# Kernel optimization log

Measured on AMD Instinct MI355X. Metric: run time of the kernel, lower is better.

The kernel has to match this reference:

```python
import jax, jax.numpy as jnp
import numpy as np
import math

B, T, C = 4, 2048, 1024
H, D = 16, 64            # num_heads, head_dim
ORIG_LEN = 4096
MIN_FREQ, MAX_FREQ = 0.5, 40.0


def setup_inputs() -> dict:
    key = jax.random.key(0)
    ks = jax.random.split(key, 6)
    x = jax.random.normal(ks[0], (B, T, C), dtype=jnp.float32)
    keep_idx = jnp.sort(jax.random.randint(ks[1], (B, T, 1), 0, ORIG_LEN), axis=1)
    W_qkv = jax.random.normal(ks[2], (C, 3 * C), dtype=jnp.float32) * (1.0 / math.sqrt(C))
    b_qkv = jnp.zeros((3 * C,), dtype=jnp.float32)
    W_proj = jax.random.normal(ks[3], (C, C), dtype=jnp.float32) * (1.0 / math.sqrt(C))
    b_proj = jnp.zeros((C,), dtype=jnp.float32)
    return {"x": x, "keep_idx": keep_idx, "original_seq_len": ORIG_LEN,
            "W_qkv": W_qkv, "b_qkv": b_qkv, "W_proj": W_proj, "b_proj": b_proj}


def _rope_angles(positions, orig_len):
    # positions: [b, t] float token positions in the ORIGINAL sequence.
    # golden_gate 1-D RoPE: normalized positions times geometric frequency band.
    half = D // 2
    freqs = MIN_FREQ * (MAX_FREQ / MIN_FREQ) ** (jnp.arange(half, dtype=jnp.float32) / (half - 1))
    pos_norm = positions / jnp.float32(orig_len)          # [b, t]
    return 2.0 * jnp.pi * pos_norm[:, :, None] * freqs    # [b, t, half]


def _apply_rope(x, cos, sin):
    # x: [b, h, t, d]; cos/sin: [b, 1, t, d/2]; rotate (first half, second half) pairs
    half = D // 2
    x1, x2 = x[..., :half], x[..., half:]
    return jnp.concatenate([x1 * cos - x2 * sin, x1 * sin + x2 * cos], axis=-1)


def reference(x, keep_idx, original_seq_len, W_qkv, b_qkv, W_proj, b_proj):
    b, t, c = x.shape
    # fused QKV projection + head split: (b,t,3c) -> (b,t,3,h,d) -> (b,h,t,3,d)
    qkv = (x @ W_qkv + b_qkv).reshape(b, t, 3, H, D).transpose(0, 3, 1, 2, 4)
    q, k, v = qkv[:, :, :, 0], qkv[:, :, :, 1], qkv[:, :, :, 2]  # each [b,h,t,d]

    positions = keep_idx[..., 0].astype(jnp.float32)             # [b, t]
    ang = _rope_angles(positions, original_seq_len)              # [b, t, d/2]
    cos = jnp.cos(ang)[:, None]                                  # [b,1,t,d/2]
    sin = jnp.sin(ang)[:, None]
    q = _apply_rope(q, cos, sin)
    k = _apply_rope(k, cos, sin)

    # dense non-causal scaled dot-product attention
    scale = 1.0 / math.sqrt(D)
    scores = jnp.einsum('bhqd,bhkd->bhqk', q, k) * scale
    attn = jax.nn.softmax(scores, axis=-1)
    out = jnp.einsum('bhqk,bhkd->bhqd', attn, v)                 # [b,h,t,d]

    out = out.transpose(0, 2, 1, 3).reshape(b, t, H * D)         # [b,t,c]
    return out @ W_proj + b_proj
```

## Files before the change

### kernel.cpp

```cpp
#include <hip/hip_runtime.h>
#include <hip/hip_bf16.h>
#include <math.h>

#define B_ 4
#define T_ 2048
#define C_ 1024
#define H_ 16
#define D_ 64

typedef __attribute__((ext_vector_type(8))) short bf16x8_t;
typedef __attribute__((ext_vector_type(4))) float f32x4_t;
typedef __attribute__((ext_vector_type(2))) unsigned int uiv2_t;

#define SHIFT2 32.0f

#define GLOAD_LDS16(gp, lp)                                                          \
    __builtin_amdgcn_global_load_lds(                                                \
        (const __attribute__((address_space(1))) void*)(gp),                         \
        (__attribute__((address_space(3))) void*)(lp), 16, 0, 0)

#define WAVE_ORDER() __builtin_amdgcn_wave_barrier()

__device__ inline unsigned int pack2bf(float a, float b) {
    __hip_bfloat162 h = __float22bfloat162_rn(make_float2(a, b));
    return *reinterpret_cast<unsigned int*>(&h);
}

__global__ __launch_bounds__(256)
void prep_kernel(const float* __restrict__ x, __hip_bfloat16* __restrict__ xbf,
                 const int* __restrict__ keep, const int* __restrict__ orig,
                 float* __restrict__ tab,
                 const float* __restrict__ Wqkv, __hip_bfloat16* __restrict__ WqkvT,
                 const float* __restrict__ Wproj, __hip_bfloat16* __restrict__ WprojT) {
    __shared__ float s[32][33];
    const int bid = blockIdx.x;
    const int tid = threadIdx.x;

    if (bid < 8192) {
        int i = bid * 256 + tid;
        float4 v = *(const float4*)(x + (size_t)i * 4);
        uint2 u;
        u.x = pack2bf(v.x, v.y);
        u.y = pack2bf(v.z, v.w);
        *(uint2*)(xbf + (size_t)i * 4) = u;
    } else if (bid < 9216) {
        int i = (bid - 8192) * 256 + tid;
        int tok = i >> 5, d = i & 31;
        float freq = 0.5f * exp2f((float)d * (6.321928094887362f / 31.0f));
        float ang  = 6.283185307179586f * ((float)keep[tok] / (float)(*orig)) * freq;
        tab[(size_t)tok * 64 + d]      = cosf(ang);
        tab[(size_t)tok * 64 + 32 + d] = sinf(ang);
    } else {
        const float* in;
        __hip_bfloat16* outp;
        int N, n0, k0, r;
        if (bid < 12288) {
            r = bid - 9216;
            in = Wqkv; outp = WqkvT; N = 3 * C_;
            n0 = (r % 96) * 32; k0 = (r / 96) * 32;
        } else {
            r = bid - 12288;
            in = Wproj; outp = WprojT; N = C_;
            n0 = (r % 32) * 32; k0 = (r / 32) * 32;
        }
        const int K = C_;
        const int tx = tid & 31;
        const int ty = tid >> 5;
#pragma unroll
        for (int yy = 0; yy < 32; yy += 8)
            s[ty + yy][tx] = in[(size_t)(k0 + ty + yy) * N + n0 + tx];
        __syncthreads();
#pragma unroll
        for (int yy = 0; yy < 32; yy += 8)
            outp[(size_t)(n0 + ty + yy) * K + k0 + tx] = __float2bfloat16(s[tx][ty + yy]);
    }
}

#define ATILE (256 * 32)
#define BTILE (128 * 32)

template <int MODE>
__global__ __launch_bounds__(512)
void gemm_kernel(const __hip_bfloat16* __restrict__ A,
                 const __hip_bfloat16* __restrict__ BT,
                 const float* __restrict__ bias,
                 float* __restrict__ out,
                 __hip_bfloat16* __restrict__ qbuf,
                 __hip_bfloat16* __restrict__ kbuf,
                 __hip_bfloat16* __restrict__ vtbuf,
                 const float* __restrict__ ropetab,
                 int M, int N, int K) {
    __shared__ __align__(16) __hip_bfloat16 GS[2 * ATILE + 2 * BTILE];

    const int tid  = threadIdx.x;
    const int lane = tid & 63;
    const int wave = tid >> 6;
    const int wm   = wave >> 1;
    const int wn   = wave & 1;
    const int l15  = lane & 15;
    const int quad = lane >> 4;

    const int nT  = N >> 7;
    const int grp = blockIdx.x / (8 * nT);
    const int rem = blockIdx.x - grp * 8 * nT;
    const int m0  = (grp * 8 + (rem & 7)) * 256;
    const int n0  = (rem >> 3) * 128;

    f32x4_t acc[4][4];
#pragma unroll
    for (int i = 0; i < 4; i++)
#pragma unroll
        for (int j = 0; j < 4; j++) acc[i][j] = (f32x4_t)0.0f;

    const int lrow = lane >> 2;
    const int scol = ((lane & 3) ^ ((lane >> 4) & 3)) * 8;
    const __hip_bfloat16* gA  = A  + (size_t)(m0 + wave * 32 + lrow) * K + scol;
    const __hip_bfloat16* gA2 = gA + (size_t)16 * K;
    const __hip_bfloat16* gB  = BT + (size_t)(n0 + wave * 16 + lrow) * K + scol;
    const int ldsA = wave * 32 * 32;
    const int ldsB = wave * 16 * 32;

    const int NK = K >> 5;
    GLOAD_LDS16(gA,  GS + ldsA);
    GLOAD_LDS16(gA2, GS + ldsA + 16 * 32);
    GLOAD_LDS16(gB,  GS + 2 * ATILE + ldsB);

    for (int t = 0; t < NK; ++t) {
        const int Ab = (t & 1) * ATILE;
        const int Bb = 2 * ATILE + (t & 1) * BTILE;
        if (t + 1 < NK) {
            const int An = (~t & 1) * ATILE;
            const int Bn = 2 * ATILE + (~t & 1) * BTILE;
            const int kk = (t + 1) << 5;
            GLOAD_LDS16(gA  + kk, GS + An + ldsA);
            GLOAD_LDS16(gA2 + kk, GS + An + ldsA + 16 * 32);
            GLOAD_LDS16(gB  + kk, GS + Bn + ldsB);
            asm volatile("s_waitcnt vmcnt(3)" ::: "memory");
        } else {
            asm volatile("s_waitcnt vmcnt(0)" ::: "memory");
        }
        __builtin_amdgcn_s_barrier();
        __builtin_amdgcn_sched_barrier(0);

        bf16x8_t af[4], bfv[4];
#pragma unroll
        for (int i = 0; i < 4; i++)
            af[i] = *(const bf16x8_t*)(GS + Ab + (wm * 64 + i * 16 + l15) * 32 +
                                       ((quad ^ (l15 >> 2)) * 8));
#pragma unroll
        for (int j = 0; j < 4; j++)
            bfv[j] = *(const bf16x8_t*)(GS + Bb + (wn * 64 + j * 16 + l15) * 32 +
                                        ((quad ^ (l15 >> 2)) * 8));
#pragma unroll
        for (int i = 0; i < 4; i++)
#pragma unroll
            for (int j = 0; j < 4; j++)
                acc[i][j] = __builtin_amdgcn_mfma_f32_16x16x32_bf16(af[i], bfv[j], acc[i][j], 0, 0, 0);

        __builtin_amdgcn_sched_barrier(0);
        asm volatile("s_waitcnt lgkmcnt(0)" ::: "memory");
        __builtin_amdgcn_s_barrier();
    }

    float bv[4];
#pragma unroll
    for (int j = 0; j < 4; j++)
        bv[j] = bias[n0 + wn * 64 + j * 16 + l15];

    if (MODE == 0) {
#pragma unroll
        for (int i = 0; i < 4; i++)
#pragma unroll
            for (int r = 0; r < 4; r++) {
                int row = m0 + wm * 64 + i * 16 + quad * 4 + r;
#pragma unroll
                for (int j = 0; j < 4; j++) {
                    int col = n0 + wn * 64 + j * 16 + l15;
                    out[(size_t)row * N + col] = acc[i][j][r] + bv[j];
                }
            }
    } else {
        const int cb   = n0 + wn * 64;
        const int part = cb >> 10;
        if (part == 2) {
            const int hb = (n0 & 1023) >> 6;
            const int bb = m0 >> 11;
            const int t0 = m0 & 2047;
            __hip_bfloat16* L = GS;
#pragma unroll
            for (int p = 0; p < 2; ++p) {
                if ((wm >> 1) == p) {
#pragma unroll
                    for (int j = 0; j < 4; j++) {
                        int d = wn * 64 + j * 16 + l15;
#pragma unroll
                        for (int i = 0; i < 4; i++) {
                            int rtb = (wm & 1) * 64 + i * 16 + quad * 4;
                            uint2 pk;
                            pk.x = pack2bf(acc[i][j][0] + bv[j], acc[i][j][1] + bv[j]);
                            pk.y = pack2bf(acc[i][j][2] + bv[j], acc[i][j][3] + bv[j]);
                            *(uint2*)(L + d * 136 + rtb) = pk;
                        }
                    }
                }
                __syncthreads();
                {
                    int row = tid >> 2;
                    int hb2 = hb + (row >> 6);
                    int dd  = row & 63;
                    const __hip_bfloat16* src = L + row * 136;
                    __hip_bfloat16* dstv = vtbuf +
                        ((size_t)((bb * H_ + hb2) * D_ + dd)) * T_ + t0 + p * 128;
#pragma unroll
                    for (int s2 = 0; s2 < 4; s2++) {
                        int ch = (tid & 3) + s2 * 4;
                        *(bf16x8_t*)(dstv + ch * 8) = *(const bf16x8_t*)(src + ch * 8);
                    }
                }
                if (p == 0) __syncthreads();
            }
        } else {
            const int h = (cb & 1023) >> 6;
            __hip_bfloat16* dst = (part == 0) ? qbuf : kbuf;
            const float sc = (part == 0) ? 0.18033688011112042f : 1.0f;
#pragma unroll
            for (int i = 0; i < 4; i++) {
#pragma unroll
                for (int r = 0; r < 4; r++) {
                    int row = m0 + wm * 64 + i * 16 + quad * 4 + r;
                    int b = row >> 11;
                    int t = row & 2047;
                    const float* trow = ropetab + (size_t)row * 64;
                    size_t base = ((size_t)(b * H_ + h) * T_ + t) * D_;
#pragma unroll
                    for (int j = 0; j < 2; j++) {
                        int d = j * 16 + l15;
                        float cs = trow[d];
                        float sn = trow[32 + d];
                        float x1 = acc[i][j][r]     + bv[j];
                        float x2 = acc[i][j + 2][r] + bv[j + 2];
                        dst[base + d]      = __float2bfloat16(sc * (x1 * cs - x2 * sn));
                        dst[base + d + 32] = __float2bfloat16(sc * (x1 * sn + x2 * cs));
                    }
                }
            }
        }
    }
}

#define KVTILE (64 * 64)

__global__ __launch_bounds__(256, 4)
void attn_kernel(const __hip_bfloat16* __restrict__ q,
                 const __hip_bfloat16* __restrict__ k,
                 const __hip_bfloat16* __restrict__ vt,
                 __hip_bfloat16* __restrict__ attn_out) {
    __shared__ __align__(16) __hip_bfloat16 SMEM[4 * KVTILE];

    const int tid  = threadIdx.x;
    const int lane = tid & 63;
    const int wave = tid >> 6;
    const int l15  = lane & 15;
    const int quad = lane >> 4;
    const int x7   = l15 & 7;

    const int bh = blockIdx.x & 63;
    const int qt = blockIdx.x >> 6;
    const int b  = bh >> 4;
    const int h  = bh & 15;

    const size_t qkbase = (size_t)bh * T_ * D_;
    const size_t vbase  = (size_t)bh * D_ * T_;
    const int    qrow0  = qt * 128 + wave * 32;

    const int drow   = lane >> 3;
    const int gchunk = (lane & 7) ^ drow;

    const __hip_bfloat16* kg = k + qkbase;
    const __hip_bfloat16* vg = vt + vbase;

    const int c0 = ((quad)     ^ x7) * 8;
    const int c1 = ((4 + quad) ^ x7) * 8;

    bf16x8_t qa[2][2];
#pragma unroll
    for (int qf = 0; qf < 2; qf++)
#pragma unroll
        for (int kk = 0; kk < 2; kk++)
            qa[qf][kk] = *(const bf16x8_t*)(q + qkbase +
                          (size_t)(qrow0 + qf * 16 + l15) * D_ + kk * 32 + quad * 8);

    bf16x8_t ones;
#pragma unroll
    for (int i = 0; i < 8; i++) ones[i] = (short)0x3F80;

    const f32x4_t mbias = (f32x4_t)(-SHIFT2);

    f32x4_t o[2][4];
#pragma unroll
    for (int qf = 0; qf < 2; qf++)
#pragma unroll
        for (int jd = 0; jd < 4; jd++) o[qf][jd] = (f32x4_t)0.0f;
    f32x4_t osum[2];
    osum[0] = (f32x4_t)0.0f;
    osum[1] = (f32x4_t)0.0f;

#pragma unroll
    for (int i = 0; i < 2; i++) {
        int r = wave * 16 + i * 8;
        GLOAD_LDS16(kg + (size_t)(r + drow) * D_ + gchunk * 8, SMEM + r * 64);
        GLOAD_LDS16(vg + (size_t)(r + drow) * T_ + gchunk * 8, SMEM + 2 * KVTILE + r * 64);
    }

    for (int kt = 0; kt < T_ / 64; kt++) {
        const int curoff = (kt & 1) * KVTILE;
        const int nxtoff = curoff ^ KVTILE;
        if (kt + 1 < T_ / 64) {
#pragma unroll
            for (int i = 0; i < 2; i++) {
                int r = wave * 16 + i * 8;
                GLOAD_LDS16(kg + (size_t)((kt + 1) * 64 + r + drow) * D_ + gchunk * 8,
                            SMEM + nxtoff + r * 64);
                GLOAD_LDS16(vg + (size_t)(r + drow) * T_ + (kt + 1) * 64 + gchunk * 8,
                            SMEM + 2 * KVTILE + nxtoff + r * 64);
            }
            asm volatile("s_waitcnt vmcnt(4)" ::: "memory");
        } else {
            asm volatile("s_waitcnt vmcnt(0)" ::: "memory");
        }
        __builtin_amdgcn_s_barrier();
        __builtin_amdgcn_sched_barrier(0);

        const __hip_bfloat16* KLc = SMEM + curoff;
        const __hip_bfloat16* VLc = SMEM + 2 * KVTILE + curoff;

        bf16x8_t kf[4][2];
#pragma unroll
        for (int jt = 0; jt < 4; jt++) {
            kf[jt][0] = *(const bf16x8_t*)(KLc + (jt * 16 + l15) * 64 + c0);
            kf[jt][1] = *(const bf16x8_t*)(KLc + (jt * 16 + l15) * 64 + c1);
        }

        f32x4_t sT[2][4];
        __builtin_amdgcn_s_setprio(1);
#pragma unroll
        for (int jt = 0; jt < 4; jt++)
#pragma unroll
            for (int qf = 0; qf < 2; qf++) {
                sT[qf][jt] = __builtin_amdgcn_mfma_f32_16x16x32_bf16(
                    kf[jt][0], qa[qf][0], mbias, 0, 0, 0);
                sT[qf][jt] = __builtin_amdgcn_mfma_f32_16x16x32_bf16(
                    kf[jt][1], qa[qf][1], sT[qf][jt], 0, 0, 0);
            }
        __builtin_amdgcn_s_setprio(0);

        bf16x8_t pb[2][2];
#pragma unroll
        for (int qf = 0; qf < 2; qf++) {
            unsigned int w0[4], w1[4];
#pragma unroll
            for (int jt = 0; jt < 4; jt++) {
                float p0 = __builtin_amdgcn_exp2f(sT[qf][jt][0]);
                float p1 = __builtin_amdgcn_exp2f(sT[qf][jt][1]);
                float p2 = __builtin_amdgcn_exp2f(sT[qf][jt][2]);
                float p3 = __builtin_amdgcn_exp2f(sT[qf][jt][3]);
                w0[jt] = pack2bf(p0, p1);
                w1[jt] = pack2bf(p2, p3);
            }
#pragma unroll
            for (int kk = 0; kk < 2; kk++) {
                uiv2_t s0 = __builtin_amdgcn_permlane32_swap(w0[2 * kk], w0[2 * kk + 1], false, false);
                uiv2_t r0 = __builtin_amdgcn_permlane16_swap(s0[0], s0[1], false, false);
                uiv2_t s1 = __builtin_amdgcn_permlane32_swap(w1[2 * kk], w1[2 * kk + 1], false, false);
                uiv2_t r1 = __builtin_amdgcn_permlane16_swap(s1[0], s1[1], false, false);
                union { unsigned int u[4]; bf16x8_t v; } pu;
                pu.u[0] = r0[0];
                pu.u[1] = r1[0];
                pu.u[2] = r0[1];
                pu.u[3] = r1[1];
                pb[qf][kk] = pu.v;
            }
        }

        __builtin_amdgcn_s_setprio(1);
#pragma unroll
        for (int qf = 0; qf < 2; qf++) {
            osum[qf] = __builtin_amdgcn_mfma_f32_16x16x32_bf16(ones, pb[qf][0], osum[qf], 0, 0, 0);
            osum[qf] = __builtin_amdgcn_mfma_f32_16x16x32_bf16(ones, pb[qf][1], osum[qf], 0, 0, 0);
        }

#pragma unroll
        for (int jd = 0; jd < 4; jd++) {
            bf16x8_t vf0 = *(const bf16x8_t*)(VLc + (jd * 16 + l15) * 64 + c0);
            bf16x8_t vf1 = *(const bf16x8_t*)(VLc + (jd * 16 + l15) * 64 + c1);
#pragma unroll
            for (int qf = 0; qf < 2; qf++) {
                o[qf][jd] = __builtin_amdgcn_mfma_f32_16x16x32_bf16(vf0, pb[qf][0], o[qf][jd], 0, 0, 0);
                o[qf][jd] = __builtin_amdgcn_mfma_f32_16x16x32_bf16(vf1, pb[qf][1], o[qf][jd], 0, 0, 0);
            }
        }
        __builtin_amdgcn_s_setprio(0);

        __builtin_amdgcn_sched_barrier(0);
        asm volatile("s_waitcnt lgkmcnt(0)" ::: "memory");
        __builtin_amdgcn_s_barrier();
    }

    float inv[2];
    inv[0] = 1.0f / osum[0][0];
    inv[1] = 1.0f / osum[1][0];

    __hip_bfloat16* Pep = SMEM + wave * (32 * 72);

    WAVE_ORDER();
#pragma unroll
    for (int qf = 0; qf < 2; qf++) {
#pragma unroll
        for (int jd = 0; jd < 4; jd++) {
            uint2 pk;
            pk.x = pack2bf(o[qf][jd][0] * inv[qf], o[qf][jd][1] * inv[qf]);
            pk.y = pack2bf(o[qf][jd][2] * inv[qf], o[qf][jd][3] * inv[qf]);
            *(uint2*)(Pep + (qf * 16 + l15) * 72 + jd * 16 + quad * 4) = pk;
        }
    }
    WAVE_ORDER();

#pragma unroll
    for (int rnd = 0; rnd < 4; rnd++) {
        int row = rnd * 8 + (lane >> 3);
        int col = (lane & 7) * 8;
        bf16x8_t vrow = *(const bf16x8_t*)(Pep + row * 72 + col);
        int token = qt * 128 + wave * 32 + row;
        *(bf16x8_t*)(attn_out + ((size_t)(b * T_ + token)) * C_ + h * 64 + col) = vrow;
    }
}

extern "C" void kernel_launch(void* const* d_in, const int* in_sizes, int n_in,
                              void* d_out, int out_size, void* d_ws, size_t ws_size,
                              hipStream_t stream) {
    const float* x        = (const float*)d_in[0];
    const int*   keep_idx = (const int*)d_in[1];
    const int*   orig_len = (const int*)d_in[2];
    const float* Wqkv     = (const float*)d_in[3];
    const float* bqkv     = (const float*)d_in[4];
    const float* Wproj    = (const float*)d_in[5];
    const float* bproj    = (const float*)d_in[6];
    float*       out      = (float*)d_out;

    const size_t NTOK = (size_t)B_ * T_;
    const size_t QKV1 = NTOK * C_;

    __hip_bfloat16* qbuf    = (__hip_bfloat16*)d_ws;
    __hip_bfloat16* kbuf    = qbuf    + QKV1;
    __hip_bfloat16* vtbuf   = kbuf    + QKV1;
    __hip_bfloat16* attnbuf = vtbuf   + QKV1;
    __hip_bfloat16* WqkvT   = attnbuf + QKV1;
    __hip_bfloat16* WprojT  = WqkvT   + (size_t)C_ * 3 * C_;
    __hip_bfloat16* xbf     = WprojT  + (size_t)C_ * C_;
    float*          ropetab = (float*)(xbf + QKV1);

    prep_kernel<<<13312, 256, 0, stream>>>(x, xbf, keep_idx, orig_len, ropetab,
                                           Wqkv, WqkvT, Wproj, WprojT);

    gemm_kernel<1><<<(8192 / 256) * (3072 / 128), 512, 0, stream>>>(
        xbf, WqkvT, bqkv, nullptr, qbuf, kbuf, vtbuf, ropetab, 8192, 3072, 1024);

    attn_kernel<<<(T_ / 128) * 64, 256, 0, stream>>>(qbuf, kbuf, vtbuf, attnbuf);

    gemm_kernel<0><<<(8192 / 256) * (1024 / 128), 512, 0, stream>>>(
        attnbuf, WprojT, bproj, out, nullptr, nullptr, nullptr, nullptr, 8192, 1024, 1024);
}
```

Baseline: 269.2 us.

## Triple-buffer GEMM tiles and drop second barrier per k-step in GEMM and attention

```diff
diff --git a/kernel.cpp b/kernel.cpp
--- a/kernel.cpp
+++ b/kernel.cpp
@@ -90,7 +90,7 @@
                  __hip_bfloat16* __restrict__ vtbuf,
                  const float* __restrict__ ropetab,
                  int M, int N, int K) {
-    __shared__ __align__(16) __hip_bfloat16 GS[2 * ATILE + 2 * BTILE];
+    __shared__ __align__(16) __hip_bfloat16 GS[3 * ATILE + 3 * BTILE];
 
     const int tid  = threadIdx.x;
     const int lane = tid & 63;
@@ -123,18 +123,17 @@
     const int NK = K >> 5;
     GLOAD_LDS16(gA,  GS + ldsA);
     GLOAD_LDS16(gA2, GS + ldsA + 16 * 32);
-    GLOAD_LDS16(gB,  GS + 2 * ATILE + ldsB);
-
+    GLOAD_LDS16(gB,  GS + 3 * ATILE + ldsB);
+    if (NK > 1) {
+        GLOAD_LDS16(gA  + 32, GS + ATILE + ldsA);
+        GLOAD_LDS16(gA2 + 32, GS + ATILE + ldsA + 16 * 32);
+        GLOAD_LDS16(gB  + 32, GS + 3 * ATILE + BTILE + ldsB);
+    }
+
+    int cur = 0;
+    int pre = 2;
     for (int t = 0; t < NK; ++t) {
-        const int Ab = (t & 1) * ATILE;
-        const int Bb = 2 * ATILE + (t & 1) * BTILE;
         if (t + 1 < NK) {
-            const int An = (~t & 1) * ATILE;
-            const int Bn = 2 * ATILE + (~t & 1) * BTILE;
-            const int kk = (t + 1) << 5;
-            GLOAD_LDS16(gA  + kk, GS + An + ldsA);
-            GLOAD_LDS16(gA2 + kk, GS + An + ldsA + 16 * 32);
-            GLOAD_LDS16(gB  + kk, GS + Bn + ldsB);
             asm volatile("s_waitcnt vmcnt(3)" ::: "memory");
         } else {
             asm volatile("s_waitcnt vmcnt(0)" ::: "memory");
@@ -142,6 +141,16 @@
         __builtin_amdgcn_s_barrier();
         __builtin_amdgcn_sched_barrier(0);
 
+        if (t + 2 < NK) {
+            const int kk = (t + 2) << 5;
+            GLOAD_LDS16(gA  + kk, GS + pre * ATILE + ldsA);
+            GLOAD_LDS16(gA2 + kk, GS + pre * ATILE + ldsA + 16 * 32);
+            GLOAD_LDS16(gB  + kk, GS + 3 * ATILE + pre * BTILE + ldsB);
+            __builtin_amdgcn_sched_barrier(0);
+        }
+
+        const int Ab = cur * ATILE;
+        const int Bb = 3 * ATILE + cur * BTILE;
         bf16x8_t af[4], bfv[4];
 #pragma unroll
         for (int i = 0; i < 4; i++)
@@ -157,9 +166,8 @@
             for (int j = 0; j < 4; j++)
                 acc[i][j] = __builtin_amdgcn_mfma_f32_16x16x32_bf16(af[i], bfv[j], acc[i][j], 0, 0, 0);
 
-        __builtin_amdgcn_sched_barrier(0);
-        asm volatile("s_waitcnt lgkmcnt(0)" ::: "memory");
-        __builtin_amdgcn_s_barrier();
+        cur = (cur == 2) ? 0 : cur + 1;
+        pre = (pre == 2) ? 0 : pre + 1;
     }
 
     float bv[4];
@@ -183,6 +191,7 @@
         const int cb   = n0 + wn * 64;
         const int part = cb >> 10;
         if (part == 2) {
+            __syncthreads();
             const int hb = (n0 & 1023) >> 6;
             const int bb = m0 >> 11;
             const int t0 = m0 & 2047;
@@ -315,6 +324,11 @@
     for (int kt = 0; kt < T_ / 64; kt++) {
         const int curoff = (kt & 1) * KVTILE;
         const int nxtoff = curoff ^ KVTILE;
+
+        asm volatile("s_waitcnt vmcnt(0)" ::: "memory");
+        __builtin_amdgcn_s_barrier();
+        __builtin_amdgcn_sched_barrier(0);
+
         if (kt + 1 < T_ / 64) {
 #pragma unroll
             for (int i = 0; i < 2; i++) {
@@ -324,12 +338,8 @@
                 GLOAD_LDS16(vg + (size_t)(r + drow) * T_ + (kt + 1) * 64 + gchunk * 8,
                             SMEM + 2 * KVTILE + nxtoff + r * 64);
             }
-            asm volatile("s_waitcnt vmcnt(4)" ::: "memory");
-        } else {
-            asm volatile("s_waitcnt vmcnt(0)" ::: "memory");
-        }
-        __builtin_amdgcn_s_barrier();
-        __builtin_amdgcn_sched_barrier(0);
+            __builtin_amdgcn_sched_barrier(0);
+        }
 
         const __hip_bfloat16* KLc = SMEM + curoff;
         const __hip_bfloat16* VLc = SMEM + 2 * KVTILE + curoff;
@@ -400,19 +410,15 @@
             }
         }
         __builtin_amdgcn_s_setprio(0);
-
-        __builtin_amdgcn_sched_barrier(0);
-        asm volatile("s_waitcnt lgkmcnt(0)" ::: "memory");
-        __builtin_amdgcn_s_barrier();
     }
 
     float inv[2];
     inv[0] = 1.0f / osum[0][0];
     inv[1] = 1.0f / osum[1][0];
 
+    __syncthreads();
     __hip_bfloat16* Pep = SMEM + wave * (32 * 72);
 
-    WAVE_ORDER();
 #pragma unroll
     for (int qf = 0; qf < 2; qf++) {
 #pragma unroll
```

Result: faster. 262.1 us (-2.6%).
